# Kernel tuning notes

Measured on AMD Instinct MI355X. Metric: run time of the kernel, lower is better.

Reference implementation:

```python
import jax, jax.numpy as jnp
import numpy as np
from jax import lax

N = 50000       # nodes
E = 1600000     # edges
D_IN = 1024     # input feature size
H = 256         # hidden size
L = 64          # GCN2Conv layers
C = 4           # n_classes
ALPHA = 0.2
THETA = 0.5


def setup_inputs() -> dict:
    key = jax.random.key(0)
    ks = jax.random.split(key, 7)
    x = jax.random.normal(ks[0], (N, D_IN), dtype=jnp.float32)
    edge_index = jax.random.randint(ks[1], (2, E), 0, N, dtype=jnp.int32)
    proj_W = jax.random.normal(ks[2], (D_IN, H), dtype=jnp.float32) * 0.02
    proj_b = jnp.zeros((H,), dtype=jnp.float32)
    weights = jax.random.normal(ks[3], (L, H, H), dtype=jnp.float32) * 0.05
    cls_W = jax.random.normal(ks[4], (H, C), dtype=jnp.float32) * 0.05
    cls_b = jnp.zeros((C,), dtype=jnp.float32)
    return {"x": x, "edge_index": edge_index, "proj_W": proj_W,
            "proj_b": proj_b, "weights": weights, "cls_W": cls_W, "cls_b": cls_b}


def reference(x, edge_index, proj_W, proj_b, weights, cls_W, cls_b):
    # Dropout is identity in eval mode (reference baseline).
    src, dst = edge_index[0], edge_index[1]
    # gcn_norm with added self-loops: A_hat = D^{-1/2} (A + I) D^{-1/2}
    loops = jnp.arange(N, dtype=src.dtype)
    src_f = jnp.concatenate([src, loops])
    dst_f = jnp.concatenate([dst, loops])
    deg = jax.ops.segment_sum(jnp.ones((E + N,), jnp.float32), dst_f, num_segments=N)
    dinv = jnp.where(deg > 0, lax.rsqrt(deg), 0.0)
    norm = dinv[src_f] * dinv[dst_f]  # [E+N]

    h0 = x @ proj_W + proj_b          # project: [N, H]
    betas = jnp.log(THETA / jnp.arange(1, L + 1, dtype=jnp.float32) + 1.0)  # [L]

    def step(h, wb):
        W, beta = wb
        # propagate: out[i] = sum_{(j->i)} norm * h[j]
        agg = jax.ops.segment_sum(norm[:, None] * h[src_f], dst_f, num_segments=N)
        s = (1.0 - ALPHA) * agg + ALPHA * h0     # initial residual
        h = (1.0 - beta) * s + beta * (s @ W)    # identity mapping (shared weights)
        return jax.nn.relu(h), None

    h, _ = lax.scan(step, h0, (weights, betas))
    out = h @ cls_W + cls_b  # classifier: [N, C]
    return out
```

## Files before the change

kernel.cpp:

```cpp
#include <hip/hip_runtime.h>
#include <math.h>

#define N_NODES 50000
#define N_EDGES 1600000
#define DIN 1024
#define H 256
#define L_LAYERS 64
#define ALPHA 0.2f

typedef unsigned short u16;
typedef short short8 __attribute__((ext_vector_type(8)));
typedef unsigned short ushort8_t __attribute__((ext_vector_type(8)));
typedef float f32x4 __attribute__((ext_vector_type(4)));
typedef unsigned int u32x4 __attribute__((ext_vector_type(4)));

__device__ inline float b2f(u16 h) { return __uint_as_float(((unsigned)h) << 16); }
__device__ inline u16 f2b(float f) {
  unsigned u = __float_as_uint(f);
  unsigned r = u + 0x7FFFu + ((u >> 16) & 1u);
  return (u16)(r >> 16);
}

__global__ void GCNIIForDialog_18923625906417_kernel() {}

__global__ __launch_bounds__(256) void k_zero(int* __restrict__ p, int n) {
  int i = blockIdx.x * 256 + threadIdx.x;
  if (i < n) p[i] = 0;
}

__global__ __launch_bounds__(256) void k_count(const int* __restrict__ dst, int* __restrict__ cnt) {
  int e = blockIdx.x * 256 + threadIdx.x;
  if (e < N_EDGES) atomicAdd(&cnt[dst[e]], 1);
}

__global__ __launch_bounds__(256) void k_dinv(const int* __restrict__ cnt, float* __restrict__ dinv) {
  int i = blockIdx.x * 256 + threadIdx.x;
  if (i < N_NODES) dinv[i] = 1.0f / sqrtf((float)(cnt[i] + 1));
}

__global__ __launch_bounds__(1024) void k_scan(const int* __restrict__ cnt, int* __restrict__ offs) {
  const int CH = (N_NODES + 1023) / 1024;
  __shared__ int sums[1024];
  int t = threadIdx.x;
  int lo = t * CH, hi = lo + CH;
  if (hi > N_NODES) hi = N_NODES;
  int s = 0;
  for (int i = lo; i < hi; ++i) s += cnt[i];
  sums[t] = s;
  __syncthreads();
  for (int d = 1; d < 1024; d <<= 1) {
    int v = (t >= d) ? sums[t - d] : 0;
    __syncthreads();
    sums[t] += v;
    __syncthreads();
  }
  int run = (t == 0) ? 0 : sums[t - 1];
  for (int i = lo; i < hi; ++i) { offs[i] = run; run += cnt[i]; }
  if (t == 0) offs[N_NODES] = sums[1023];
}

__global__ __launch_bounds__(256) void k_scatter(const int* __restrict__ src, const int* __restrict__ dst,
    const int* __restrict__ offs, int* __restrict__ cursor, const float* __restrict__ dinv,
    int* __restrict__ col, float* __restrict__ w) {
  int e = blockIdx.x * 256 + threadIdx.x;
  if (e >= N_EDGES) return;
  int sN = src[e], dN = dst[e];
  int pos = offs[dN] + atomicAdd(&cursor[dN], 1);
  col[pos] = sN;
  w[pos] = dinv[sN] * dinv[dN];
}

__global__ void k_wtr(const float* __restrict__ Win, u16* __restrict__ Wout) {
  __shared__ float tile[32][33];
  size_t base = (size_t)blockIdx.z * H * H;
  int n0 = blockIdx.x * 32, k0 = blockIdx.y * 32;
  for (int i = threadIdx.y; i < 32; i += 8)
    tile[i][threadIdx.x] = Win[base + (size_t)(k0 + i) * H + n0 + threadIdx.x];
  __syncthreads();
  for (int i = threadIdx.y; i < 32; i += 8)
    Wout[base + (size_t)(n0 + i) * H + k0 + threadIdx.x] = f2b(tile[threadIdx.x][i]);
}

__global__ void k_trP(const float* __restrict__ Win, u16* __restrict__ Wout) {
  __shared__ float tile[32][33];
  int n0 = blockIdx.x * 32, k0 = blockIdx.y * 32;
  for (int i = threadIdx.y; i < 32; i += 8)
    tile[i][threadIdx.x] = Win[(size_t)(k0 + i) * H + n0 + threadIdx.x];
  __syncthreads();
  for (int i = threadIdx.y; i < 32; i += 8)
    Wout[(size_t)(n0 + i) * DIN + k0 + threadIdx.x] = f2b(tile[threadIdx.x][i]);
}

__global__ __launch_bounds__(256) void k_spmm(
    const u16* __restrict__ h, const u16* __restrict__ h0b,
    const int* __restrict__ offs, const int* __restrict__ col, const float* __restrict__ w,
    const float* __restrict__ dinv, u16* __restrict__ sb)
{
  int wid = threadIdx.x >> 6, lane = threadIdx.x & 63;
  int node = blockIdx.x * 4 + wid;
  if (node >= N_NODES) return;
  int half = lane >> 5;
  int c8 = (lane & 31) * 8;
  float acc[8] = {0.f, 0.f, 0.f, 0.f, 0.f, 0.f, 0.f, 0.f};
  if (half == 0) {
    float di = dinv[node];
    float di2 = di * di;
    ushort8_t hv = *(const ushort8_t*)(h + (size_t)node * H + c8);
#pragma unroll
    for (int k = 0; k < 8; ++k) acc[k] = di2 * b2f(hv[k]);
  }
  int base = offs[node];
  int d = offs[node + 1] - base;
  int i = half;
  for (; i + 2 < d; i += 4) {
    int e0 = base + i, e1 = base + i + 2;
    int j0 = col[e0], j1 = col[e1];
    float w0 = w[e0], w1 = w[e1];
    ushort8_t v0 = *(const ushort8_t*)(h + (size_t)j0 * H + c8);
    ushort8_t v1 = *(const ushort8_t*)(h + (size_t)j1 * H + c8);
#pragma unroll
    for (int k = 0; k < 8; ++k) acc[k] += w0 * b2f(v0[k]);
#pragma unroll
    for (int k = 0; k < 8; ++k) acc[k] += w1 * b2f(v1[k]);
  }
  for (; i < d; i += 2) {
    int e0 = base + i;
    int j0 = col[e0];
    float w0 = w[e0];
    ushort8_t v0 = *(const ushort8_t*)(h + (size_t)j0 * H + c8);
#pragma unroll
    for (int k = 0; k < 8; ++k) acc[k] += w0 * b2f(v0[k]);
  }
#pragma unroll
  for (int k = 0; k < 8; ++k) acc[k] += __shfl_xor(acc[k], 32);
  if (half == 0) {
    ushort8_t h0v = *(const ushort8_t*)(h0b + (size_t)node * H + c8);
    ushort8_t o;
#pragma unroll
    for (int k = 0; k < 8; ++k)
      o[k] = f2b((1.0f - ALPHA) * acc[k] + ALPHA * b2f(h0v[k]));
    *(ushort8_t*)(sb + (size_t)node * H + c8) = o;
  }
}

__global__ __launch_bounds__(256) void k_gemm(
    const u16* __restrict__ A, const u16* __restrict__ BT,
    u16* __restrict__ Hout, float beta)
{
  __shared__ u16 As[128 * 40];
  __shared__ u16 Bs[128 * 40];
  int tid = threadIdx.x;
  int mBase = blockIdx.x * 128, nBase = blockIdx.y * 128;
  int wid = tid >> 6, lane = tid & 63;
  int wm = (wid & 1) * 64, wn = (wid >> 1) * 64;
  int lrow = lane & 15, quad = lane >> 4;
  f32x4 acc[4][4] = {};
  int sr = tid >> 2, sc = tid & 3;
  for (int k0 = 0; k0 < H; k0 += 32) {
#pragma unroll
    for (int it = 0; it < 2; ++it) {
      int r = sr + it * 64;
      int grow = mBase + r;
      u32x4 va = {};
      if (grow < N_NODES) va = *(const u32x4*)(A + (size_t)grow * H + k0 + sc * 8);
      *(u32x4*)&As[r * 40 + sc * 8] = va;
      u32x4 vb = *(const u32x4*)(BT + (size_t)(nBase + r) * H + k0 + sc * 8);
      *(u32x4*)&Bs[r * 40 + sc * 8] = vb;
    }
    __syncthreads();
    short8 af[4], bfr[4];
#pragma unroll
    for (int i = 0; i < 4; ++i) {
      af[i]  = *(const short8*)&As[(wm + i * 16 + lrow) * 40 + quad * 8];
      bfr[i] = *(const short8*)&Bs[(wn + i * 16 + lrow) * 40 + quad * 8];
    }
#pragma unroll
    for (int mi = 0; mi < 4; ++mi)
#pragma unroll
      for (int ni = 0; ni < 4; ++ni)
        acc[mi][ni] = __builtin_amdgcn_mfma_f32_16x16x32_bf16(af[mi], bfr[ni], acc[mi][ni], 0, 0, 0);
    __syncthreads();
  }
#pragma unroll
  for (int mi = 0; mi < 4; ++mi)
#pragma unroll
    for (int ni = 0; ni < 4; ++ni)
#pragma unroll
      for (int rg = 0; rg < 4; ++rg) {
        int r = mBase + wm + mi * 16 + quad * 4 + rg;
        int c = nBase + wn + ni * 16 + lrow;
        if (r < N_NODES) {
          size_t idx = (size_t)r * H + c;
          float v = (1.0f - beta) * b2f(A[idx]) + beta * acc[mi][ni][rg];
          Hout[idx] = f2b(fmaxf(v, 0.0f));
        }
      }
}

__global__ __launch_bounds__(256) void k_pgemm(
    const float* __restrict__ X, const u16* __restrict__ BT,
    const float* __restrict__ bias, u16* __restrict__ h0b, u16* __restrict__ h)
{
  __shared__ u16 As[128 * 40];
  __shared__ u16 Bs[128 * 40];
  int tid = threadIdx.x;
  int mBase = blockIdx.x * 128, nBase = blockIdx.y * 128;
  int wid = tid >> 6, lane = tid & 63;
  int wm = (wid & 1) * 64, wn = (wid >> 1) * 64;
  int lrow = lane & 15, quad = lane >> 4;
  f32x4 acc[4][4] = {};
  int sr = tid >> 2, sc = tid & 3;
  for (int k0 = 0; k0 < DIN; k0 += 32) {
#pragma unroll
    for (int it = 0; it < 2; ++it) {
      int r = sr + it * 64;
      int grow = mBase + r;
      float4 fa0 = make_float4(0.f, 0.f, 0.f, 0.f);
      float4 fa1 = make_float4(0.f, 0.f, 0.f, 0.f);
      if (grow < N_NODES) {
        const float* ap = X + (size_t)grow * DIN + k0 + sc * 8;
        fa0 = *(const float4*)ap;
        fa1 = *(const float4*)(ap + 4);
      }
      ushort8_t av;
      av[0] = f2b(fa0.x); av[1] = f2b(fa0.y); av[2] = f2b(fa0.z); av[3] = f2b(fa0.w);
      av[4] = f2b(fa1.x); av[5] = f2b(fa1.y); av[6] = f2b(fa1.z); av[7] = f2b(fa1.w);
      *(ushort8_t*)&As[r * 40 + sc * 8] = av;
      u32x4 vb = *(const u32x4*)(BT + (size_t)(nBase + r) * DIN + k0 + sc * 8);
      *(u32x4*)&Bs[r * 40 + sc * 8] = vb;
    }
    __syncthreads();
    short8 af[4], bfr[4];
#pragma unroll
    for (int i = 0; i < 4; ++i) {
      af[i]  = *(const short8*)&As[(wm + i * 16 + lrow) * 40 + quad * 8];
      bfr[i] = *(const short8*)&Bs[(wn + i * 16 + lrow) * 40 + quad * 8];
    }
#pragma unroll
    for (int mi = 0; mi < 4; ++mi)
#pragma unroll
      for (int ni = 0; ni < 4; ++ni)
        acc[mi][ni] = __builtin_amdgcn_mfma_f32_16x16x32_bf16(af[mi], bfr[ni], acc[mi][ni], 0, 0, 0);
    __syncthreads();
  }
#pragma unroll
  for (int mi = 0; mi < 4; ++mi)
#pragma unroll
    for (int ni = 0; ni < 4; ++ni)
#pragma unroll
      for (int rg = 0; rg < 4; ++rg) {
        int r = mBase + wm + mi * 16 + quad * 4 + rg;
        int c = nBase + wn + ni * 16 + lrow;
        if (r < N_NODES) {
          size_t idx = (size_t)r * H + c;
          float v = acc[mi][ni][rg] + bias[c];
          u16 bv = f2b(v);
          h0b[idx] = bv;
          h[idx] = bv;
        }
      }
}

__global__ __launch_bounds__(256) void k_cls(const u16* __restrict__ h,
    const float* __restrict__ W, const float* __restrict__ b, float* __restrict__ out)
{
  int wid = threadIdx.x >> 6, lane = threadIdx.x & 63;
  int node = blockIdx.x * 4 + wid;
  if (node >= N_NODES) return;
  float a0 = 0, a1 = 0, a2 = 0, a3 = 0;
  for (int t = lane; t < H; t += 64) {
    float hv = b2f(h[(size_t)node * H + t]);
    a0 += hv * W[t * 4 + 0];
    a1 += hv * W[t * 4 + 1];
    a2 += hv * W[t * 4 + 2];
    a3 += hv * W[t * 4 + 3];
  }
#pragma unroll
  for (int off = 32; off > 0; off >>= 1) {
    a0 += __shfl_down(a0, off);
    a1 += __shfl_down(a1, off);
    a2 += __shfl_down(a2, off);
    a3 += __shfl_down(a3, off);
  }
  if (lane == 0) {
    float4 o;
    o.x = a0 + b[0];
    o.y = a1 + b[1];
    o.z = a2 + b[2];
    o.w = a3 + b[3];
    *(float4*)(out + (size_t)node * 4) = o;
  }
}

extern "C" void kernel_launch(void* const* d_in, const int* in_sizes, int n_in,
                              void* d_out, int out_size, void* d_ws, size_t ws_size,
                              hipStream_t stream) {
  (void)in_sizes; (void)n_in; (void)out_size; (void)ws_size;
  const float* x     = (const float*)d_in[0];
  const int*   ei    = (const int*)d_in[1];
  const float* projW = (const float*)d_in[2];
  const float* projB = (const float*)d_in[3];
  const float* wts   = (const float*)d_in[4];
  const float* clsW  = (const float*)d_in[5];
  const float* clsB  = (const float*)d_in[6];
  float* out = (float*)d_out;

  char* ws = (char*)d_ws;
  size_t off = 0;
  auto alloc = [&](size_t bytes) -> void* {
    void* p = ws + off;
    off = (off + bytes + 255) & ~(size_t)255;
    return p;
  };
  int*   cntcur = (int*)alloc((size_t)N_NODES * 2 * 4);
  int*   cnt    = cntcur;
  int*   cursor = cntcur + N_NODES;
  int*   offs   = (int*)alloc((size_t)(N_NODES + 1) * 4);
  float* dinv   = (float*)alloc((size_t)N_NODES * 4);
  int*   col    = (int*)alloc((size_t)N_EDGES * 4);
  float* w      = (float*)alloc((size_t)N_EDGES * 4);
  u16*   WT     = (u16*)alloc((size_t)L_LAYERS * H * H * 2);
  u16*   BTp    = (u16*)alloc((size_t)H * DIN * 2);
  u16*   h0b    = (u16*)alloc((size_t)N_NODES * H * 2);
  u16*   sb     = (u16*)alloc((size_t)N_NODES * H * 2);
  u16*   h      = (u16*)alloc((size_t)N_NODES * H * 2);

  const int* src = ei;
  const int* dst = ei + N_EDGES;

  k_zero<<<(N_NODES * 2 + 255) / 256, 256, 0, stream>>>(cntcur, N_NODES * 2);
  k_count<<<(N_EDGES + 255) / 256, 256, 0, stream>>>(dst, cnt);
  k_dinv<<<(N_NODES + 255) / 256, 256, 0, stream>>>(cnt, dinv);
  k_scan<<<1, 1024, 0, stream>>>(cnt, offs);
  k_scatter<<<(N_EDGES + 255) / 256, 256, 0, stream>>>(src, dst, offs, cursor, dinv, col, w);
  k_wtr<<<dim3(H / 32, H / 32, L_LAYERS), dim3(32, 8), 0, stream>>>(wts, WT);
  k_trP<<<dim3(H / 32, DIN / 32), dim3(32, 8), 0, stream>>>(projW, BTp);

  k_pgemm<<<dim3((N_NODES + 127) / 128, H / 128), 256, 0, stream>>>(x, BTp, projB, h0b, h);

  dim3 ggrid((N_NODES + 127) / 128, H / 128);
  for (int l = 0; l < L_LAYERS; ++l) {
    k_spmm<<<(N_NODES + 3) / 4, 256, 0, stream>>>(h, h0b, offs, col, w, dinv, sb);
    float beta = logf(0.5f / (float)(l + 1) + 1.0f);
    k_gemm<<<ggrid, 256, 0, stream>>>(sb, WT + (size_t)l * H * H, h, beta);
  }
  k_cls<<<(N_NODES + 3) / 4, 256, 0, stream>>>(h, clsW, clsB, out);
}
```

Measured before the change: 10.44 ms.

## Store features in column-chunked layout and split SpMM across column chunks

Node features are stored as 8 column-chunks of 32 bf16 columns each, laid out chunk-major, so that each SpMM block gathers only a 64-byte slice per neighbor and the working set per chunk fits better in cache. Each wave now handles 16 edges in parallel with 4 lanes per edge, reducing across lanes by shuffles. Edge index and weight are packed into a single int2 array. The GEMM, projection and classifier kernels are updated to the new layout. This trades 8x more SpMM blocks and repeated reads of edge lists per chunk for better locality of the gathers.

```diff
diff --git a/kernel.cpp b/kernel.cpp
--- a/kernel.cpp
+++ b/kernel.cpp
@@ -7,6 +7,8 @@
 #define H 256
 #define L_LAYERS 64
 #define ALPHA 0.2f
+#define NCHUNK 8
+#define CCOLS 32
 
 typedef unsigned short u16;
 typedef short short8 __attribute__((ext_vector_type(8)));
@@ -19,6 +21,10 @@
   unsigned u = __float_as_uint(f);
   unsigned r = u + 0x7FFFu + ((u >> 16) & 1u);
   return (u16)(r >> 16);
+}
+
+__device__ inline size_t bidx(int node, int col) {
+  return ((size_t)(col >> 5) * N_NODES + node) * CCOLS + (col & 31);
 }
 
 __global__ void GCNIIForDialog_18923625906417_kernel() {}
@@ -61,13 +67,12 @@
 
 __global__ __launch_bounds__(256) void k_scatter(const int* __restrict__ src, const int* __restrict__ dst,
     const int* __restrict__ offs, int* __restrict__ cursor, const float* __restrict__ dinv,
-    int* __restrict__ col, float* __restrict__ w) {
+    int2* __restrict__ ew) {
   int e = blockIdx.x * 256 + threadIdx.x;
   if (e >= N_EDGES) return;
   int sN = src[e], dN = dst[e];
   int pos = offs[dN] + atomicAdd(&cursor[dN], 1);
-  col[pos] = sN;
-  w[pos] = dinv[sN] * dinv[dN];
+  ew[pos] = make_int2(sN, __float_as_int(dinv[sN] * dinv[dN]));
 }
 
 __global__ void k_wtr(const float* __restrict__ Win, u16* __restrict__ Wout) {
@@ -92,54 +97,43 @@
 }
 
 __global__ __launch_bounds__(256) void k_spmm(
-    const u16* __restrict__ h, const u16* __restrict__ h0b,
-    const int* __restrict__ offs, const int* __restrict__ col, const float* __restrict__ w,
-    const float* __restrict__ dinv, u16* __restrict__ sb)
+    const u16* __restrict__ hb, const u16* __restrict__ h0b,
+    const int* __restrict__ offs, const int2* __restrict__ ew,
+    const float* __restrict__ dinv, u16* __restrict__ sbb)
 {
+  int bid = blockIdx.x;
+  int chunk = bid & 7;
+  int nb = bid >> 3;
   int wid = threadIdx.x >> 6, lane = threadIdx.x & 63;
-  int node = blockIdx.x * 4 + wid;
+  int node = nb * 4 + wid;
   if (node >= N_NODES) return;
-  int half = lane >> 5;
-  int c8 = (lane & 31) * 8;
+  int sub = lane & 3;
+  int eoff = lane >> 2;
+  const u16* hc = hb + (size_t)chunk * N_NODES * CCOLS;
   float acc[8] = {0.f, 0.f, 0.f, 0.f, 0.f, 0.f, 0.f, 0.f};
-  if (half == 0) {
+  int base = offs[node], end = offs[node + 1];
+  for (int i = base + eoff; i < end; i += 16) {
+    int2 cw = ew[i];
+    float wv = __int_as_float(cw.y);
+    ushort8_t v = *(const ushort8_t*)(hc + (size_t)cw.x * CCOLS + sub * 8);
+#pragma unroll
+    for (int k = 0; k < 8; ++k) acc[k] += wv * b2f(v[k]);
+  }
+#pragma unroll
+  for (int d = 4; d < 64; d <<= 1)
+#pragma unroll
+    for (int k = 0; k < 8; ++k) acc[k] += __shfl_xor(acc[k], d);
+  if (eoff == 0) {
     float di = dinv[node];
     float di2 = di * di;
-    ushort8_t hv = *(const ushort8_t*)(h + (size_t)node * H + c8);
-#pragma unroll
-    for (int k = 0; k < 8; ++k) acc[k] = di2 * b2f(hv[k]);
-  }
-  int base = offs[node];
-  int d = offs[node + 1] - base;
-  int i = half;
-  for (; i + 2 < d; i += 4) {
-    int e0 = base + i, e1 = base + i + 2;
-    int j0 = col[e0], j1 = col[e1];
-    float w0 = w[e0], w1 = w[e1];
-    ushort8_t v0 = *(const ushort8_t*)(h + (size_t)j0 * H + c8);
-    ushort8_t v1 = *(const ushort8_t*)(h + (size_t)j1 * H + c8);
-#pragma unroll
-    for (int k = 0; k < 8; ++k) acc[k] += w0 * b2f(v0[k]);
-#pragma unroll
-    for (int k = 0; k < 8; ++k) acc[k] += w1 * b2f(v1[k]);
-  }
-  for (; i < d; i += 2) {
-    int e0 = base + i;
-    int j0 = col[e0];
-    float w0 = w[e0];
-    ushort8_t v0 = *(const ushort8_t*)(h + (size_t)j0 * H + c8);
-#pragma unroll
-    for (int k = 0; k < 8; ++k) acc[k] += w0 * b2f(v0[k]);
-  }
-#pragma unroll
-  for (int k = 0; k < 8; ++k) acc[k] += __shfl_xor(acc[k], 32);
-  if (half == 0) {
-    ushort8_t h0v = *(const ushort8_t*)(h0b + (size_t)node * H + c8);
+    size_t ci = (size_t)chunk * N_NODES * CCOLS + (size_t)node * CCOLS + sub * 8;
+    ushort8_t hv = *(const ushort8_t*)(hc + (size_t)node * CCOLS + sub * 8);
+    ushort8_t h0v = *(const ushort8_t*)(h0b + ci);
     ushort8_t o;
 #pragma unroll
     for (int k = 0; k < 8; ++k)
-      o[k] = f2b((1.0f - ALPHA) * acc[k] + ALPHA * b2f(h0v[k]));
-    *(ushort8_t*)(sb + (size_t)node * H + c8) = o;
+      o[k] = f2b((1.0f - ALPHA) * (acc[k] + di2 * b2f(hv[k])) + ALPHA * b2f(h0v[k]));
+    *(ushort8_t*)(sbb + ci) = o;
   }
 }
 
@@ -157,12 +151,13 @@
   f32x4 acc[4][4] = {};
   int sr = tid >> 2, sc = tid & 3;
   for (int k0 = 0; k0 < H; k0 += 32) {
+    const u16* Ac = A + (size_t)(k0 >> 5) * N_NODES * CCOLS;
 #pragma unroll
     for (int it = 0; it < 2; ++it) {
       int r = sr + it * 64;
       int grow = mBase + r;
       u32x4 va = {};
-      if (grow < N_NODES) va = *(const u32x4*)(A + (size_t)grow * H + k0 + sc * 8);
+      if (grow < N_NODES) va = *(const u32x4*)(Ac + (size_t)grow * CCOLS + sc * 8);
       *(u32x4*)&As[r * 40 + sc * 8] = va;
       u32x4 vb = *(const u32x4*)(BT + (size_t)(nBase + r) * H + k0 + sc * 8);
       *(u32x4*)&Bs[r * 40 + sc * 8] = vb;
@@ -190,7 +185,7 @@
         int r = mBase + wm + mi * 16 + quad * 4 + rg;
         int c = nBase + wn + ni * 16 + lrow;
         if (r < N_NODES) {
-          size_t idx = (size_t)r * H + c;
+          size_t idx = bidx(r, c);
           float v = (1.0f - beta) * b2f(A[idx]) + beta * acc[mi][ni][rg];
           Hout[idx] = f2b(fmaxf(v, 0.0f));
         }
@@ -252,7 +247,7 @@
         int r = mBase + wm + mi * 16 + quad * 4 + rg;
         int c = nBase + wn + ni * 16 + lrow;
         if (r < N_NODES) {
-          size_t idx = (size_t)r * H + c;
+          size_t idx = bidx(r, c);
           float v = acc[mi][ni][rg] + bias[c];
           u16 bv = f2b(v);
           h0b[idx] = bv;
@@ -269,7 +264,7 @@
   if (node >= N_NODES) return;
   float a0 = 0, a1 = 0, a2 = 0, a3 = 0;
   for (int t = lane; t < H; t += 64) {
-    float hv = b2f(h[(size_t)node * H + t]);
+    float hv = b2f(h[bidx(node, t)]);
     a0 += hv * W[t * 4 + 0];
     a1 += hv * W[t * 4 + 1];
     a2 += hv * W[t * 4 + 2];
@@ -317,8 +312,7 @@
   int*   cursor = cntcur + N_NODES;
   int*   offs   = (int*)alloc((size_t)(N_NODES + 1) * 4);
   float* dinv   = (float*)alloc((size_t)N_NODES * 4);
-  int*   col    = (int*)alloc((size_t)N_EDGES * 4);
-  float* w      = (float*)alloc((size_t)N_EDGES * 4);
+  int2*  ew     = (int2*)alloc((size_t)N_EDGES * 8);
   u16*   WT     = (u16*)alloc((size_t)L_LAYERS * H * H * 2);
   u16*   BTp    = (u16*)alloc((size_t)H * DIN * 2);
   u16*   h0b    = (u16*)alloc((size_t)N_NODES * H * 2);
@@ -332,15 +326,16 @@
   k_count<<<(N_EDGES + 255) / 256, 256, 0, stream>>>(dst, cnt);
   k_dinv<<<(N_NODES + 255) / 256, 256, 0, stream>>>(cnt, dinv);
   k_scan<<<1, 1024, 0, stream>>>(cnt, offs);
-  k_scatter<<<(N_EDGES + 255) / 256, 256, 0, stream>>>(src, dst, offs, cursor, dinv, col, w);
+  k_scatter<<<(N_EDGES + 255) / 256, 256, 0, stream>>>(src, dst, offs, cursor, dinv, ew);
   k_wtr<<<dim3(H / 32, H / 32, L_LAYERS), dim3(32, 8), 0, stream>>>(wts, WT);
   k_trP<<<dim3(H / 32, DIN / 32), dim3(32, 8), 0, stream>>>(projW, BTp);
 
   k_pgemm<<<dim3((N_NODES + 127) / 128, H / 128), 256, 0, stream>>>(x, BTp, projB, h0b, h);
 
   dim3 ggrid((N_NODES + 127) / 128, H / 128);
+  const int spmm_blocks = ((N_NODES + 3) / 4) * NCHUNK;
   for (int l = 0; l < L_LAYERS; ++l) {
-    k_spmm<<<(N_NODES + 3) / 4, 256, 0, stream>>>(h, h0b, offs, col, w, dinv, sb);
+    k_spmm<<<spmm_blocks, 256, 0, stream>>>(h, h0b, offs, ew, dinv, sb);
     float beta = logf(0.5f / (float)(l + 1) + 1.0f);
     k_gemm<<<ggrid, 256, 0, stream>>>(sb, WT + (size_t)l * H * H, h, beta);
   }
```

Result: slower. 14.30 ms (+37.0%).
